# Performance work log

Measured on AMD Instinct MI355X. Metric: run time of the kernel, lower is better.

The kernel has to match this reference:

```python
import jax, jax.numpy as jnp
import numpy as np

B, N, GEO, CLS = 32, 1024, 4, 28
F0 = GEO + CLS          # 32
F1 = F0 * 2             # 64
F2 = F0 * 4             # 128
EPS = 1e-5


def _lin(x, W, b):
    return x @ W.T + b


def _bn(x, g, b):
    # torch BatchNorm1d(element_num) on [B, N, F]: channel dim is N,
    # normalize over (batch, feature) with biased variance (training mode).
    m = x.mean(axis=(0, 2), keepdims=True)
    v = ((x - m) ** 2).mean(axis=(0, 2), keepdims=True)
    return g[None, :, None] * (x - m) * jax.lax.rsqrt(v + EPS) + b[None, :, None]


def _relation(x, Wu, bu, psi, phi, wr):
    # Vectorized form of the triple python loop:
    #   S[b,i,j] = psi*phi * <x_i, x_j>, diagonal excluded
    #   out_i   = wr * (sum_j S[b,i,j] * relu(unary(x_j))) / N + x_i
    n = x.shape[1]
    U = jax.nn.relu(_lin(x, Wu, bu))                       # [B,N,F2]
    S = (psi[0] * phi[0]) * jnp.einsum('bnd,bmd->bnm', x, x)
    S = S * (1.0 - jnp.eye(n, dtype=x.dtype))              # mask i==j
    return wr[0] * (S @ U) / n + x


def setup_inputs() -> dict:
    key = jax.random.key(0)
    ks = iter(jax.random.split(key, 64))

    def W(o, i):
        return jax.random.normal(next(ks), (o, i), jnp.float32) * 0.02

    def bvec(o):
        return jnp.zeros((o,), jnp.float32)

    inp = {'input': jax.random.uniform(next(ks), (B, N, F0), jnp.float32)}
    inp.update(e1_W=W(F1, F0), e1_b=bvec(F1),
               bn1_g=jnp.ones((N,), jnp.float32), bn1_b=bvec(N),
               e2_W=W(F2, F1), e2_b=bvec(F2),
               bn2_g=jnp.ones((N,), jnp.float32), bn2_b=bvec(N),
               e3_W=W(F2, F2), e3_b=bvec(F2))
    for r in (1, 2, 3, 4):
        inp[f'r{r}_W'] = W(F2, F2)
        inp[f'r{r}_b'] = bvec(F2)
        inp[f'r{r}_psi'] = jax.random.uniform(next(ks), (1,), jnp.float32)
        inp[f'r{r}_phi'] = jax.random.uniform(next(ks), (1,), jnp.float32)
        inp[f'r{r}_wr'] = jax.random.uniform(next(ks), (1,), jnp.float32)
    inp.update(d1_W=W(F1, F2), d1_b=bvec(F1),
               dbn_g=jnp.ones((N,), jnp.float32), dbn_b=bvec(N),
               d2_W=W(F0, F1), d2_b=bvec(F0),
               bc_W=W(CLS, F0), bc_b=bvec(CLS),
               bg_W=W(GEO, F0), bg_b=bvec(GEO))
    return inp


def reference(input, e1_W, e1_b, bn1_g, bn1_b, e2_W, e2_b, bn2_g, bn2_b,
              e3_W, e3_b,
              r1_W, r1_b, r1_psi, r1_phi, r1_wr,
              r2_W, r2_b, r2_psi, r2_phi, r2_wr,
              r3_W, r3_b, r3_psi, r3_phi, r3_wr,
              r4_W, r4_b, r4_psi, r4_phi, r4_wr,
              d1_W, d1_b, dbn_g, dbn_b, d2_W, d2_b,
              bc_W, bc_b, bg_W, bg_b):
    out = jax.nn.relu(_bn(_lin(input, e1_W, e1_b), bn1_g, bn1_b))
    out = jax.nn.relu(_bn(_lin(out, e2_W, e2_b), bn2_g, bn2_b))
    enc = jax.nn.sigmoid(_lin(out, e3_W, e3_b))
    x = _relation(enc, r1_W, r1_b, r1_psi, r1_phi, r1_wr)
    x = _relation(x, r2_W, r2_b, r2_psi, r2_phi, r2_wr)
    x = _relation(x, r3_W, r3_b, r3_psi, r3_phi, r3_wr)
    x = _relation(x, r4_W, r4_b, r4_psi, r4_phi, r4_wr)
    out = jax.nn.relu(_bn(_lin(x, d1_W, d1_b), dbn_g, dbn_b))
    out = jax.nn.relu(_lin(out, d2_W, d2_b))
    syn_cls = _lin(out, bc_W, bc_b)
    syn_geo = _lin(out, bg_W, bg_b)
    return jnp.concatenate((syn_cls, syn_geo), axis=2)
```

## Files before the change

### kernel.cpp

```cpp
#include <hip/hip_runtime.h>
#include <hip/hip_bf16.h>


typedef __hip_bfloat16 bf16;
typedef unsigned short ushort_t;
typedef float v4f __attribute__((ext_vector_type(4)));
typedef short v8s __attribute__((ext_vector_type(8)));
#define MFMA_BF16 __builtin_amdgcn_mfma_f32_16x16x32_bf16

#define NB 32
#define NN 1024

__device__ __forceinline__ float ldin(const void* p, size_t i, int f32){
    return f32 ? ((const float*)p)[i] : __bfloat162float(((const bf16*)p)[i]);
}
__device__ __forceinline__ float bf2f(ushort_t u){
    return __uint_as_float((unsigned)u << 16);
}
__device__ __forceinline__ ushort_t f2bf(float v){
    bf16 h = __float2bfloat16(v);
    ushort_t s; __builtin_memcpy(&s, &h, 2);
    return s;
}
__device__ __forceinline__ void unpack8(uint4 v, float* f){
    f[0] = __uint_as_float(v.x << 16);
    f[1] = __uint_as_float(v.x & 0xffff0000u);
    f[2] = __uint_as_float(v.y << 16);
    f[3] = __uint_as_float(v.y & 0xffff0000u);
    f[4] = __uint_as_float(v.z << 16);
    f[5] = __uint_as_float(v.z & 0xffff0000u);
    f[6] = __uint_as_float(v.w << 16);
    f[7] = __uint_as_float(v.w & 0xffff0000u);
}

__device__ __forceinline__ int detect_dev(const void* inp){
    __shared__ int sflag;
    int t = threadIdx.x;
    if (t < 64){
        unsigned v = ((const unsigned*)inp)[t];
        unsigned long long m = __ballot((v & 0x80008000u) != 0u);
        if (t == 0) sflag = (__popcll(m) > 4) ? 1 : 0;
    }
    __syncthreads();
    return sflag;
}

struct PrepArgs {
    const void* w[11];
    int K[11], O[11], off[11];
};

__global__ __launch_bounds__(256) void k_prep(PrepArgs a, float* __restrict__ wpf,
                                              ushort_t* __restrict__ whi, ushort_t* __restrict__ wlo,
                                              const void* __restrict__ detin){
    int f32 = detect_dev(detin);
    int s = blockIdx.y;
    int idx = blockIdx.x*256 + threadIdx.x;
    if (s < 6){
        int K = a.K[s], O = a.O[s];
        if (idx >= K*O) return;
        int k = idx / O, j = idx - k*O;
        wpf[a.off[s] + idx] = ldin(a.w[s], (size_t)j*K + k, f32);
    } else {
        if (idx >= 16384) return;
        int n = idx >> 7, k = idx & 127;
        float v = ldin(a.w[s], (size_t)n*128 + k, f32);
        ushort_t h = f2bf(v);
        ushort_t l = f2bf(v - bf2f(h));
        int di = (s - 6)*16384 + ((k >> 3)*128 + n)*8 + (k & 7);
        whi[di] = h; wlo[di] = l;
    }
}

template<int K, int O, bool EXTIN>
__global__ __launch_bounds__(128) void k_bnlin(
    const void* __restrict__ xin, const float* __restrict__ Wt,
    const void* __restrict__ bias, const void* __restrict__ bng,
    const void* __restrict__ bnb, ushort_t* __restrict__ out,
    const void* __restrict__ detin)
{
    int f32 = detect_dev(detin);
    constexpr int BR  = O/16;
    constexpr int NBT = 32/BR;
    constexpr int G   = K/8;
    __shared__ __align__(16) float wt[K*O];
    __shared__ __align__(16) float xst[2][K*36];
    int t = threadIdx.x;
    int w = t >> 6, lane = t & 63;
    int n = blockIdx.x*2 + w;

    for (int i = t; i < K*O/4; i += 128)
        ((float4*)wt)[i] = ((const float4*)Wt)[i];
    for (int i = lane; i < 32*G; i += 64){
        int b = i / G, g = i - b*G;
        float f[8];
        if (EXTIN && f32){
            const float* src = (const float*)xin + ((size_t)b*NN + n)*K + g*8;
            float4 v0 = ((const float4*)src)[0];
            float4 v1 = ((const float4*)src)[1];
            f[0]=v0.x; f[1]=v0.y; f[2]=v0.z; f[3]=v0.w;
            f[4]=v1.x; f[5]=v1.y; f[6]=v1.z; f[7]=v1.w;
        } else {
            uint4 v = *(const uint4*)((const ushort_t*)xin + ((size_t)b*NN + n)*K + (size_t)g*8);
            unpack8(v, f);
        }
        #pragma unroll
        for (int j=0;j<8;j++) xst[w][(g*8+j)*36 + b] = f[j];
    }
    __syncthreads();

    int bt = lane % NBT, jt = lane / NBT;
    int b0 = bt*BR, j0 = jt*8;
    const float* xw = xst[w];
    float acc[BR][8];
    #pragma unroll
    for (int i=0;i<BR;i++)
        #pragma unroll
        for (int j=0;j<8;j++) acc[i][j] = 0.f;

    for (int k = 0; k < K; k++){
        float xv[BR], wv[8];
        #pragma unroll
        for (int i=0;i<BR;i+=4)
            *(float4*)&xv[i] = *(const float4*)&xw[k*36 + b0 + i];
        *(float4*)&wv[0] = *(const float4*)&wt[k*O + j0];
        *(float4*)&wv[4] = *(const float4*)&wt[k*O + j0 + 4];
        #pragma unroll
        for (int i=0;i<BR;i++)
            #pragma unroll
            for (int j=0;j<8;j++) acc[i][j] = fmaf(xv[i], wv[j], acc[i][j]);
    }

    float bj[8];
    #pragma unroll
    for (int j=0;j<8;j++) bj[j] = ldin(bias, j0+j, f32);
    float s1 = 0.f, s2 = 0.f;
    #pragma unroll
    for (int i=0;i<BR;i++)
        #pragma unroll
        for (int j=0;j<8;j++){
            float a = acc[i][j] + bj[j];
            acc[i][j] = a; s1 += a; s2 = fmaf(a, a, s2);
        }
    #pragma unroll
    for (int off = 32; off > 0; off >>= 1){
        s1 += __shfl_down(s1, off);
        s2 += __shfl_down(s2, off);
    }
    s1 = __shfl(s1, 0); s2 = __shfl(s2, 0);
    const float M = 32.f * O;
    float m  = s1 / M;
    float vv = s2 / M - m*m;
    float rs = rsqrtf(vv + 1e-5f);
    float gv = ldin(bng, n, f32), bv = ldin(bnb, n, f32);
    #pragma unroll
    for (int i=0;i<BR;i++){
        union { uint4 u; ushort_t s[8]; } pk;
        #pragma unroll
        for (int j=0;j<8;j++)
            pk.s[j] = f2bf(fmaxf(fmaf(gv*(acc[i][j]-m), rs, bv), 0.f));
        *(uint4*)(out + ((size_t)(b0+i)*NN + n)*O + j0) = pk.u;
    }
}



__device__ __forceinline__ void tail_stage_x(ushort_t* xs, const float o[2][16],
                                             int w, int col, int quad){
    #pragma unroll
    for (int nt=0;nt<2;nt++){
        int n = w*32 + nt*16 + col;
        #pragma unroll
        for (int m=0;m<4;m++)
            #pragma unroll
            for (int reg=0;reg<4;reg++){
                int r = m*16 + quad*4 + reg;
                xs[((n>>3)*64 + r)*8 + (n&7)] = f2bf(o[nt][m*4+reg]);
            }
    }
}

__device__ __forceinline__ void tail_write_A(const ushort_t* xs, ushort_t* A,
                                             size_t row0, int t){
    uint4* dst = (uint4*)(A + row0*128);
    #pragma unroll
    for (int c = 0; c < 4; c++){
        int i = t + c*256;
        int r = i >> 4, kg = i & 15;
        dst[i] = *(const uint4*)&xs[(kg*64 + r)*8];
    }
}

__device__ __forceinline__ void tail_lin_relu(ushort_t* xs, ushort_t* UT,
    const ushort_t* Whi, const ushort_t* Wlo, const void* bias, float* dvec,
    size_t row0, int b, int rbase, int t, int w, int lane, int col, int quad, int f32)
{
    if (t < 64){
        float s = 0.f;
        #pragma unroll 8
        for (int k=0;k<128;k++){
            float v = bf2f(xs[((k>>3)*64 + t)*8 + (k&7)]);
            s = fmaf(v, v, s);
        }
        dvec[row0 + t] = s;
    }
    v4f acc[4][2];
    #pragma unroll
    for (int m=0;m<4;m++)
        #pragma unroll
        for (int nt=0;nt<2;nt++) acc[m][nt] = (v4f){0.f,0.f,0.f,0.f};
    #pragma unroll
    for (int kt = 0; kt < 4; kt++){
        int kg = kt*4 + quad;
        v8s a[4], bh[2], bl[2];
        #pragma unroll
        for (int nt=0;nt<2;nt++){
            int n = w*32 + nt*16 + col;
            bh[nt] = *(const v8s*)&Whi[(kg*128 + n)*8];
            bl[nt] = *(const v8s*)&Wlo[(kg*128 + n)*8];
        }
        #pragma unroll
        for (int m=0;m<4;m++)
            a[m] = *(const v8s*)&xs[(kg*64 + m*16 + col)*8];
        #pragma unroll
        for (int m=0;m<4;m++)
            #pragma unroll
            for (int nt=0;nt<2;nt++){
                acc[m][nt] = MFMA_BF16(a[m], bh[nt], acc[m][nt], 0, 0, 0);
                acc[m][nt] = MFMA_BF16(a[m], bl[nt], acc[m][nt], 0, 0, 0);
            }
    }
    float u[2][16];
    #pragma unroll
    for (int nt=0;nt<2;nt++){
        int n = w*32 + nt*16 + col;
        float bn = ldin(bias, n, f32);
        #pragma unroll
        for (int m=0;m<4;m++)
            #pragma unroll
            for (int reg=0;reg<4;reg++)
                u[nt][m*4+reg] = fmaxf(acc[m][nt][reg] + bn, 0.f);
    }
    __syncthreads();
    #pragma unroll
    for (int nt=0;nt<2;nt++){
        int n = w*32 + nt*16 + col;
        #pragma unroll
        for (int m=0;m<4;m++)
            #pragma unroll
            for (int reg=0;reg<4;reg++){
                int r = m*16 + quad*4 + reg;
                xs[n*64 + r] = f2bf(u[nt][m*4+reg]);
            }
    }
    __syncthreads();
    #pragma unroll
    for (int c = 0; c < 4; c++){
        int i = t + c*256;
        int n = i >> 3, sg = i & 7;
        *(uint4*)&UT[((size_t)b*128 + n)*1024 + rbase + sg*8] =
            *(const uint4*)&xs[n*64 + sg*8];
    }
}

__global__ __launch_bounds__(256, 2) void k_linfuse0(
    const ushort_t* __restrict__ xin,
    const ushort_t* __restrict__ W3h, const ushort_t* __restrict__ W3l,
    const void* __restrict__ b3,
    const ushort_t* __restrict__ W1h, const ushort_t* __restrict__ W1l,
    const void* __restrict__ b1,
    ushort_t* __restrict__ A, ushort_t* __restrict__ UT,
    float* __restrict__ dvec, const void* __restrict__ detin)
{
    __shared__ __align__(16) ushort_t xs[8192];
    int f32 = detect_dev(detin);
    int t = threadIdx.x;
    size_t row0 = (size_t)blockIdx.x * 64;
    int b = (int)(row0 >> 10), rbase = (int)(row0 & 1023);
    {
        const uint4* src = (const uint4*)(xin + row0*128);
        #pragma unroll
        for (int c = 0; c < 4; c++){
            int i = t + c*256;
            int r = i >> 4, kg = i & 15;
            *(uint4*)&xs[(kg*64 + r)*8] = src[i];
        }
    }
    __syncthreads();
    int w = t >> 6, lane = t & 63;
    int col = lane & 15, quad = lane >> 4;
    v4f acc[4][2];
    #pragma unroll
    for (int m=0;m<4;m++)
        #pragma unroll
        for (int nt=0;nt<2;nt++) acc[m][nt] = (v4f){0.f,0.f,0.f,0.f};
    #pragma unroll
    for (int kt = 0; kt < 4; kt++){
        int kg = kt*4 + quad;
        v8s a[4], bh[2], bl[2];
        #pragma unroll
        for (int nt=0;nt<2;nt++){
            int n = w*32 + nt*16 + col;
            bh[nt] = *(const v8s*)&W3h[(kg*128 + n)*8];
            bl[nt] = *(const v8s*)&W3l[(kg*128 + n)*8];
        }
        #pragma unroll
        for (int m=0;m<4;m++)
            a[m] = *(const v8s*)&xs[(kg*64 + m*16 + col)*8];
        #pragma unroll
        for (int m=0;m<4;m++)
            #pragma unroll
            for (int nt=0;nt<2;nt++){
                acc[m][nt] = MFMA_BF16(a[m], bh[nt], acc[m][nt], 0, 0, 0);
                acc[m][nt] = MFMA_BF16(a[m], bl[nt], acc[m][nt], 0, 0, 0);
            }
    }
    float o[2][16];
    #pragma unroll
    for (int nt=0;nt<2;nt++){
        int n = w*32 + nt*16 + col;
        float bn = ldin(b3, n, f32);
        #pragma unroll
        for (int m=0;m<4;m++)
            #pragma unroll
            for (int reg=0;reg<4;reg++){
                float v = acc[m][nt][reg] + bn;
                o[nt][m*4+reg] = 1.f/(1.f+expf(-v));
            }
    }
    __syncthreads();
    tail_stage_x(xs, o, w, col, quad);
    __syncthreads();
    tail_write_A(xs, A, row0, t);
    tail_lin_relu(xs, UT, W1h, W1l, b1, dvec, row0, b, rbase, t, w, lane, col, quad, f32);
}

__global__ __launch_bounds__(256) void k_relT(
    const ushort_t* __restrict__ x, const ushort_t* __restrict__ UT,
    float* __restrict__ Tp)
{
    __shared__ __align__(16) ushort_t xts[8192];
    int blk = blockIdx.x;
    int b = blk & 31, rs = (blk >> 5) & 7, nh = blk >> 8;
    int t = threadIdx.x;
    int w = t >> 6, lane = t & 63;
    int col = lane & 15, quad = lane >> 4;
    int wn = nh*64 + (w & 1)*32;
    int wc = (w >> 1)*64;
    const ushort_t* utb = UT + ((size_t)b << 17);
    v4f acc[2][4];
    #pragma unroll
    for (int m=0;m<2;m++)
        #pragma unroll
        for (int q=0;q<4;q++) acc[m][q] = (v4f){0.f,0.f,0.f,0.f};

    for (int ch = 0; ch < 2; ch++){
        __syncthreads();
        int r0 = rs*128 + ch*64;
        #pragma unroll
        for (int c = 0; c < 4; c++){
            int i = t + c*256;
            int r = i >> 4, cs8 = (i & 15)*8;
            uint4 v = *(const uint4*)&x[((size_t)b*1024 + r0 + r)*128 + cs8];
            int base = ((r >> 3)*128 + cs8)*8 + (r & 7);
            xts[base     ] = (ushort_t)(v.x & 0xffff);
            xts[base + 8 ] = (ushort_t)(v.x >> 16);
            xts[base + 16] = (ushort_t)(v.y & 0xffff);
            xts[base + 24] = (ushort_t)(v.y >> 16);
            xts[base + 32] = (ushort_t)(v.z & 0xffff);
            xts[base + 40] = (ushort_t)(v.z >> 16);
            xts[base + 48] = (ushort_t)(v.w & 0xffff);
            xts[base + 56] = (ushort_t)(v.w >> 16);
        }
        __syncthreads();
        #pragma unroll
        for (int kt = 0; kt < 2; kt++){
            int kg = kt*4 + quad;
            v8s a[2], bb[4];
            #pragma unroll
            for (int m=0;m<2;m++)
                a[m] = *(const v8s*)&utb[((size_t)(wn + m*16 + col))*1024 + r0 + kg*8];
            #pragma unroll
            for (int q=0;q<4;q++)
                bb[q] = *(const v8s*)&xts[(kg*128 + wc + q*16 + col)*8];
            #pragma unroll
            for (int m=0;m<2;m++)
                #pragma unroll
                for (int q=0;q<4;q++)
                    acc[m][q] = MFMA_BF16(a[m], bb[q], acc[m][q], 0, 0, 0);
        }
    }
    float* dst = Tp + (((size_t)rs*NB + b) << 14);
    #pragma unroll
    for (int m=0;m<2;m++)
        #pragma unroll
        for (int q=0;q<4;q++)
            #pragma unroll
            for (int reg=0;reg<4;reg++){
                int n = wn + m*16 + quad*4 + reg;
                int c = wc + q*16 + col;
                dst[n*128 + c] = acc[m][q][reg];
            }
}

__global__ __launch_bounds__(256) void k_tred(const float* __restrict__ Tp,
                                              ushort_t* __restrict__ Thi, ushort_t* __restrict__ Tlo){
    int i = blockIdx.x*256 + threadIdx.x;
    const size_t S = 524288;
    float s = ((Tp[i] + Tp[S+i]) + (Tp[2*S+i] + Tp[3*S+i]))
            + ((Tp[4*S+i] + Tp[5*S+i]) + (Tp[6*S+i] + Tp[7*S+i]));
    int bb = i >> 14, j = i & 16383;
    int n = j >> 7, c = j & 127;
    int di = (bb << 14) + ((c >> 3)*128 + n)*8 + (c & 7);
    ushort_t h = f2bf(s);
    Thi[di] = h;
    Tlo[di] = f2bf(s - bf2f(h));
}

template<int LAST>
__global__ __launch_bounds__(256, 2) void k_relfuse(
    ushort_t* __restrict__ x, ushort_t* __restrict__ UT,
    const ushort_t* __restrict__ Thi, const ushort_t* __restrict__ Tlo,
    float* __restrict__ dvec,
    const void* __restrict__ psi, const void* __restrict__ phi, const void* __restrict__ wr,
    const ushort_t* __restrict__ Wnh, const ushort_t* __restrict__ Wnl,
    const void* __restrict__ bnext, const void* __restrict__ detin)
{
    __shared__ __align__(16) ushort_t xs[8192];
    int f32 = detect_dev(detin);
    int t = threadIdx.x;
    size_t row0 = (size_t)blockIdx.x * 64;
    int b = (int)(row0 >> 10), rbase = (int)(row0 & 1023);
    {
        const uint4* src = (const uint4*)(x + row0*128);
        #pragma unroll
        for (int c = 0; c < 4; c++){
            int i = t + c*256;
            int r = i >> 4, kg = i & 15;
            *(uint4*)&xs[(kg*64 + r)*8] = src[i];
        }
    }
    __syncthreads();
    float alpha = ldin(wr,0,f32) * ldin(psi,0,f32) * ldin(phi,0,f32) * (1.f/1024.f);
    int w = t >> 6, lane = t & 63;
    int col = lane & 15, quad = lane >> 4;
    const ushort_t* sh = Thi + ((size_t)b << 14);
    const ushort_t* sl = Tlo + ((size_t)b << 14);
    v4f acc[4][2];
    #pragma unroll
    for (int m=0;m<4;m++)
        #pragma unroll
        for (int nt=0;nt<2;nt++) acc[m][nt] = (v4f){0.f,0.f,0.f,0.f};
    #pragma unroll
    for (int kt = 0; kt < 4; kt++){
        int kg = kt*4 + quad;
        v8s a[4], bh[2], bl[2];
        #pragma unroll
        for (int nt=0;nt<2;nt++){
            int n = w*32 + nt*16 + col;
            bh[nt] = *(const v8s*)&sh[(kg*128 + n)*8];
            bl[nt] = *(const v8s*)&sl[(kg*128 + n)*8];
        }
        #pragma unroll
        for (int m=0;m<4;m++)
            a[m] = *(const v8s*)&xs[(kg*64 + m*16 + col)*8];
        #pragma unroll
        for (int m=0;m<4;m++)
            #pragma unroll
            for (int nt=0;nt<2;nt++){
                acc[m][nt] = MFMA_BF16(a[m], bh[nt], acc[m][nt], 0, 0, 0);
                acc[m][nt] = MFMA_BF16(a[m], bl[nt], acc[m][nt], 0, 0, 0);
            }
    }
    float o[2][16];
    #pragma unroll
    for (int m=0;m<4;m++){
        float4 d4 = *(const float4*)&dvec[row0 + m*16 + quad*4];
        const float* dr = (const float*)&d4;
        #pragma unroll
        for (int nt=0;nt<2;nt++){
            int n = w*32 + nt*16 + col;
            uint2 uu = *(const uint2*)&UT[((size_t)b*128 + n)*1024 + rbase + m*16 + quad*4];
            float uf[4];
            uf[0] = __uint_as_float(uu.x << 16);
            uf[1] = __uint_as_float(uu.x & 0xffff0000u);
            uf[2] = __uint_as_float(uu.y << 16);
            uf[3] = __uint_as_float(uu.y & 0xffff0000u);
            #pragma unroll
            for (int reg=0;reg<4;reg++){
                int r = m*16 + quad*4 + reg;
                float xv = bf2f(xs[((n>>3)*64 + r)*8 + (n&7)]);
                o[nt][m*4+reg] = fmaf(alpha, acc[m][nt][reg] - dr[reg]*uf[reg], xv);
            }
        }
    }
    __syncthreads();
    tail_stage_x(xs, o, w, col, quad);
    __syncthreads();
    tail_write_A(xs, x, row0, t);
    if (!LAST)
        tail_lin_relu(xs, UT, Wnh, Wnl, bnext, dvec, row0, b, rbase, t, w, lane, col, quad, f32);
}

__global__ __launch_bounds__(256) void k_dec2(
    const ushort_t* __restrict__ x,
    const float* __restrict__ W2t, const void* __restrict__ b2,
    const float* __restrict__ Wct, const void* __restrict__ bcb,
    const float* __restrict__ Wgt, const void* __restrict__ bgb,
    void* __restrict__ out, const void* __restrict__ detin)
{
    int f32 = detect_dev(detin);
    __shared__ __align__(16) float w2[64*32];
    __shared__ __align__(16) float wc[32*28];
    __shared__ __align__(16) float wg[32*4];
    __shared__ __align__(16) float xsd[8][64];
    __shared__ float hs[8][33];
    size_t row0 = (size_t)blockIdx.x * 8;
    int t = threadIdx.x;
    for (int i=t;i<512;i+=256)  ((float4*)w2)[i] = ((const float4*)W2t)[i];
    if (t < 224) ((float4*)wc)[t] = ((const float4*)Wct)[t];
    if (t < 32)  ((float4*)wg)[t] = ((const float4*)Wgt)[t];
    if (t < 64){
        int row = t >> 3, seg = t & 7;
        uint4 v = *(const uint4*)&x[(row0 + row)*64 + seg*8];
        float f[8]; unpack8(v, f);
        *(float4*)&xsd[row][seg*8]   = make_float4(f[0],f[1],f[2],f[3]);
        *(float4*)&xsd[row][seg*8+4] = make_float4(f[4],f[5],f[6],f[7]);
    }
    __syncthreads();
    int j = t & 31, r = t >> 5;
    float a = ldin(b2, j, f32);
    #pragma unroll 8
    for (int k=0;k<64;k++) a = fmaf(xsd[r][k], w2[k*32 + j], a);
    hs[r][j] = fmaxf(a, 0.f);
    __syncthreads();
    float o;
    if (j < 28){
        o = ldin(bcb, j, f32);
        #pragma unroll
        for (int k=0;k<32;k++) o = fmaf(hs[r][k], wc[k*28 + j], o);
    } else {
        int jj = j - 28;
        o = ldin(bgb, jj, f32);
        #pragma unroll
        for (int k=0;k<32;k++) o = fmaf(hs[r][k], wg[k*4 + jj], o);
    }
    size_t oi = (row0 + r)*32 + j;
    if (f32) ((float*)out)[oi] = o;
    else     ((ushort_t*)out)[oi] = f2bf(o);
}

enum { O_E1=0, O_E2=2048, O_D1=10240, O_D2=18432, O_BC=20480, O_BG=21376 };

extern "C" void kernel_launch(void* const* d_in, const int* in_sizes, int n_in,
                              void* d_out, int out_size, void* d_ws, size_t ws_size,
                              hipStream_t stream)
{
    (void)in_sizes; (void)n_in; (void)out_size; (void)ws_size;
    const void* input = d_in[0];
    const void* e1_W = d_in[1];  const void* e1_b = d_in[2];
    const void* bn1_g = d_in[3]; const void* bn1_b = d_in[4];
    const void* e2_W = d_in[5];  const void* e2_b = d_in[6];
    const void* bn2_g = d_in[7]; const void* bn2_b = d_in[8];
    const void* e3_W = d_in[9];  const void* e3_b = d_in[10];
    const void *rW[4], *rb[4], *rpsi[4], *rphi[4], *rwr[4];
    for (int r = 0; r < 4; r++){
        rW[r]   = d_in[11 + r*5 + 0];
        rb[r]   = d_in[11 + r*5 + 1];
        rpsi[r] = d_in[11 + r*5 + 2];
        rphi[r] = d_in[11 + r*5 + 3];
        rwr[r]  = d_in[11 + r*5 + 4];
    }
    const void* d1_W = d_in[31]; const void* d1_b = d_in[32];
    const void* dbn_g = d_in[33];const void* dbn_b = d_in[34];
    const void* d2_W = d_in[35]; const void* d2_b = d_in[36];
    const void* bc_W = d_in[37]; const void* bc_b = d_in[38];
    const void* bg_W = d_in[39]; const void* bg_b = d_in[40];

    float*    ws_f = (float*)d_ws;
    float*    wpf  = ws_f;
    float*    dd   = ws_f + 21504;
    ushort_t* whi  = (ushort_t*)(ws_f + 54272);
    ushort_t* wlo  = (ushort_t*)(ws_f + 95232);
    ushort_t* Thi  = (ushort_t*)(ws_f + 136192);
    ushort_t* Tlo  = (ushort_t*)(ws_f + 398336);
    float*    Tp   = ws_f + 660480;
    ushort_t* A    = (ushort_t*)(ws_f + 4854784);
    ushort_t* UT   = (ushort_t*)(ws_f + 6951936);
    ushort_t* Cenc = A;
    ushort_t* E2   = (ushort_t*)Tp;
    ushort_t* Cdec = UT;

    PrepArgs pa;
    const void* srcs[11] = {e1_W, e2_W, d1_W, d2_W, bc_W, bg_W,
                            e3_W, rW[0], rW[1], rW[2], rW[3]};
    const int  Ks[11]   = {32,64,128,64,32,32, 128,128,128,128,128};
    const int  Os[11]   = {64,128,64,32,28,4,  128,128,128,128,128};
    const int  offs[11] = {O_E1,O_E2,O_D1,O_D2,O_BC,O_BG, 0,0,0,0,0};
    for (int i=0;i<11;i++){ pa.w[i]=srcs[i]; pa.K[i]=Ks[i]; pa.O[i]=Os[i]; pa.off[i]=offs[i]; }

    k_prep<<<dim3(64,11), 256, 0, stream>>>(pa, wpf, whi, wlo, input);
    k_bnlin<32,64,true><<<512, 128, 0, stream>>>(input, wpf+O_E1, e1_b, bn1_g, bn1_b, Cenc, input);
    k_bnlin<64,128,false><<<512, 128, 0, stream>>>(Cenc, wpf+O_E2, e2_b, bn2_g, bn2_b, E2, input);
    k_linfuse0<<<512, 256, 0, stream>>>(E2, whi, wlo, e3_b,
                                        whi + 16384, wlo + 16384, rb[0],
                                        A, UT, dd, input);

    for (int r = 0; r < 4; r++){
        k_relT<<<512, 256, 0, stream>>>(A, UT, Tp);
        k_tred<<<2048, 256, 0, stream>>>(Tp, Thi, Tlo);
        if (r < 3)
            k_relfuse<0><<<512, 256, 0, stream>>>(A, UT, Thi, Tlo, dd,
                rpsi[r], rphi[r], rwr[r],
                whi + (size_t)(2+r)*16384, wlo + (size_t)(2+r)*16384, rb[r+1], input);
        else
            k_relfuse<1><<<512, 256, 0, stream>>>(A, UT, Thi, Tlo, dd,
                rpsi[r], rphi[r], rwr[r], whi, wlo, rb[r], input);
    }

    k_bnlin<128,64,false><<<512, 128, 0, stream>>>(A, wpf+O_D1, d1_b, dbn_g, dbn_b, Cdec, input);
    k_dec2<<<4096, 256, 0, stream>>>(Cdec, wpf+O_D2, d2_b, wpf+O_BC, bc_b, wpf+O_BG, bg_b, d_out, input);
}
```

Baseline: 346.3 us.

## Fuse relation T-partial GEMM into producer tails, drop separate k_relT kernel

The U^T·x partial product for each 64-row slab is now computed in the tail of k_linfuse0/k_relfuse, using the x and U tiles already staged in shared memory (a second transposed x tile is added). This removes a separate k_relT launch and its reload of x and UT from global memory. k_tred now reduces 16 partials instead of 8, so Tp doubles in size and the workspace layout is moved. Shared memory per block doubles and the 2-blocks-per-CU launch bound is dropped, which may reduce occupancy.

```diff
diff --git a/kernel.cpp b/kernel.cpp
--- a/kernel.cpp
+++ b/kernel.cpp
@@ -164,19 +164,24 @@
 }
 
 
-
-__device__ __forceinline__ void tail_stage_x(ushort_t* xs, const float o[2][16],
+__device__ __forceinline__ void tail_stage_x(ushort_t* xs, ushort_t* xt,
+                                             const float o[2][16],
                                              int w, int col, int quad){
     #pragma unroll
     for (int nt=0;nt<2;nt++){
         int n = w*32 + nt*16 + col;
         #pragma unroll
-        for (int m=0;m<4;m++)
+        for (int m=0;m<4;m++){
+            union { uint2 u2; ushort_t s[4]; } pk;
             #pragma unroll
             for (int reg=0;reg<4;reg++){
                 int r = m*16 + quad*4 + reg;
-                xs[((n>>3)*64 + r)*8 + (n&7)] = f2bf(o[nt][m*4+reg]);
+                ushort_t hv = f2bf(o[nt][m*4+reg]);
+                xs[((n>>3)*64 + r)*8 + (n&7)] = hv;
+                pk.s[reg] = hv;
             }
+            *(uint2*)&xt[n*64 + m*16 + quad*4] = pk.u2;
+        }
     }
 }
 
@@ -191,9 +196,10 @@
     }
 }
 
-__device__ __forceinline__ void tail_lin_relu(ushort_t* xs, ushort_t* UT,
-    const ushort_t* Whi, const ushort_t* Wlo, const void* bias, float* dvec,
-    size_t row0, int b, int rbase, int t, int w, int lane, int col, int quad, int f32)
+__device__ __forceinline__ void tail_lin_relu_T(ushort_t* xs, ushort_t* xt,
+    ushort_t* UT, const ushort_t* Whi, const ushort_t* Wlo, const void* bias,
+    float* dvec, float* Tp,
+    size_t row0, int b, int rbase, int t, int w, int col, int quad, int f32)
 {
     if (t < 64){
         float s = 0.f;
@@ -246,12 +252,13 @@
     for (int nt=0;nt<2;nt++){
         int n = w*32 + nt*16 + col;
         #pragma unroll
-        for (int m=0;m<4;m++)
-            #pragma unroll
-            for (int reg=0;reg<4;reg++){
-                int r = m*16 + quad*4 + reg;
-                xs[n*64 + r] = f2bf(u[nt][m*4+reg]);
-            }
+        for (int m=0;m<4;m++){
+            union { uint2 u2; ushort_t s[4]; } pk;
+            #pragma unroll
+            for (int reg=0;reg<4;reg++)
+                pk.s[reg] = f2bf(u[nt][m*4+reg]);
+            *(uint2*)&xs[n*64 + m*16 + quad*4] = pk.u2;
+        }
     }
     __syncthreads();
     #pragma unroll
@@ -261,18 +268,54 @@
         *(uint4*)&UT[((size_t)b*128 + n)*1024 + rbase + sg*8] =
             *(const uint4*)&xs[n*64 + sg*8];
     }
-}
-
-__global__ __launch_bounds__(256, 2) void k_linfuse0(
+    v4f tacc[4][4];
+    #pragma unroll
+    for (int m=0;m<4;m++)
+        #pragma unroll
+        for (int q=0;q<4;q++) tacc[m][q] = (v4f){0.f,0.f,0.f,0.f};
+    int wn = (w & 1)*64, wc = (w >> 1)*64;
+    #pragma unroll
+    for (int kt = 0; kt < 2; kt++){
+        int kg = kt*4 + quad;
+        v8s a[4], bb[4];
+        #pragma unroll
+        for (int m=0;m<4;m++)
+            a[m] = *(const v8s*)&xs[(wn + m*16 + col)*64 + kg*8];
+        #pragma unroll
+        for (int q=0;q<4;q++)
+            bb[q] = *(const v8s*)&xt[(wc + q*16 + col)*64 + kg*8];
+        #pragma unroll
+        for (int m=0;m<4;m++)
+            #pragma unroll
+            for (int q=0;q<4;q++)
+                tacc[m][q] = MFMA_BF16(a[m], bb[q], tacc[m][q], 0, 0, 0);
+    }
+    int s16 = (int)((row0 >> 6) & 15);
+    float* dst = Tp + ((size_t)(s16*NB + b) << 14);
+    #pragma unroll
+    for (int m=0;m<4;m++)
+        #pragma unroll
+        for (int q=0;q<4;q++)
+            #pragma unroll
+            for (int reg=0;reg<4;reg++){
+                int n = wn + m*16 + quad*4 + reg;
+                int c = wc + q*16 + col;
+                dst[n*128 + c] = tacc[m][q][reg];
+            }
+}
+
+__global__ __launch_bounds__(256) void k_linfuse0(
     const ushort_t* __restrict__ xin,
     const ushort_t* __restrict__ W3h, const ushort_t* __restrict__ W3l,
     const void* __restrict__ b3,
     const ushort_t* __restrict__ W1h, const ushort_t* __restrict__ W1l,
     const void* __restrict__ b1,
     ushort_t* __restrict__ A, ushort_t* __restrict__ UT,
-    float* __restrict__ dvec, const void* __restrict__ detin)
+    float* __restrict__ dvec, float* __restrict__ Tp,
+    const void* __restrict__ detin)
 {
     __shared__ __align__(16) ushort_t xs[8192];
+    __shared__ __align__(16) ushort_t xt[8192];
     int f32 = detect_dev(detin);
     int t = threadIdx.x;
     size_t row0 = (size_t)blockIdx.x * 64;
@@ -329,86 +372,20 @@
             }
     }
     __syncthreads();
-    tail_stage_x(xs, o, w, col, quad);
+    tail_stage_x(xs, xt, o, w, col, quad);
     __syncthreads();
     tail_write_A(xs, A, row0, t);
-    tail_lin_relu(xs, UT, W1h, W1l, b1, dvec, row0, b, rbase, t, w, lane, col, quad, f32);
-}
-
-__global__ __launch_bounds__(256) void k_relT(
-    const ushort_t* __restrict__ x, const ushort_t* __restrict__ UT,
-    float* __restrict__ Tp)
-{
-    __shared__ __align__(16) ushort_t xts[8192];
-    int blk = blockIdx.x;
-    int b = blk & 31, rs = (blk >> 5) & 7, nh = blk >> 8;
-    int t = threadIdx.x;
-    int w = t >> 6, lane = t & 63;
-    int col = lane & 15, quad = lane >> 4;
-    int wn = nh*64 + (w & 1)*32;
-    int wc = (w >> 1)*64;
-    const ushort_t* utb = UT + ((size_t)b << 17);
-    v4f acc[2][4];
-    #pragma unroll
-    for (int m=0;m<2;m++)
-        #pragma unroll
-        for (int q=0;q<4;q++) acc[m][q] = (v4f){0.f,0.f,0.f,0.f};
-
-    for (int ch = 0; ch < 2; ch++){
-        __syncthreads();
-        int r0 = rs*128 + ch*64;
-        #pragma unroll
-        for (int c = 0; c < 4; c++){
-            int i = t + c*256;
-            int r = i >> 4, cs8 = (i & 15)*8;
-            uint4 v = *(const uint4*)&x[((size_t)b*1024 + r0 + r)*128 + cs8];
-            int base = ((r >> 3)*128 + cs8)*8 + (r & 7);
-            xts[base     ] = (ushort_t)(v.x & 0xffff);
-            xts[base + 8 ] = (ushort_t)(v.x >> 16);
-            xts[base + 16] = (ushort_t)(v.y & 0xffff);
-            xts[base + 24] = (ushort_t)(v.y >> 16);
-            xts[base + 32] = (ushort_t)(v.z & 0xffff);
-            xts[base + 40] = (ushort_t)(v.z >> 16);
-            xts[base + 48] = (ushort_t)(v.w & 0xffff);
-            xts[base + 56] = (ushort_t)(v.w >> 16);
-        }
-        __syncthreads();
-        #pragma unroll
-        for (int kt = 0; kt < 2; kt++){
-            int kg = kt*4 + quad;
-            v8s a[2], bb[4];
-            #pragma unroll
-            for (int m=0;m<2;m++)
-                a[m] = *(const v8s*)&utb[((size_t)(wn + m*16 + col))*1024 + r0 + kg*8];
-            #pragma unroll
-            for (int q=0;q<4;q++)
-                bb[q] = *(const v8s*)&xts[(kg*128 + wc + q*16 + col)*8];
-            #pragma unroll
-            for (int m=0;m<2;m++)
-                #pragma unroll
-                for (int q=0;q<4;q++)
-                    acc[m][q] = MFMA_BF16(a[m], bb[q], acc[m][q], 0, 0, 0);
-        }
-    }
-    float* dst = Tp + (((size_t)rs*NB + b) << 14);
-    #pragma unroll
-    for (int m=0;m<2;m++)
-        #pragma unroll
-        for (int q=0;q<4;q++)
-            #pragma unroll
-            for (int reg=0;reg<4;reg++){
-                int n = wn + m*16 + quad*4 + reg;
-                int c = wc + q*16 + col;
-                dst[n*128 + c] = acc[m][q][reg];
-            }
+    tail_lin_relu_T(xs, xt, UT, W1h, W1l, b1, dvec, Tp,
+                    row0, b, rbase, t, w, col, quad, f32);
 }
 
 __global__ __launch_bounds__(256) void k_tred(const float* __restrict__ Tp,
                                               ushort_t* __restrict__ Thi, ushort_t* __restrict__ Tlo){
     int i = blockIdx.x*256 + threadIdx.x;
     const size_t S = 524288;
-    float s = ((Tp[i] + Tp[S+i]) + (Tp[2*S+i] + Tp[3*S+i]))
-            + ((Tp[4*S+i] + Tp[5*S+i]) + (Tp[6*S+i] + Tp[7*S+i]));
+    float s = 0.f;
+    #pragma unroll
+    for (int k = 0; k < 16; k++) s += Tp[(size_t)k*S + i];
     int bb = i >> 14, j = i & 16383;
     int n = j >> 7, c = j & 127;
     int di = (bb << 14) + ((c >> 3)*128 + n)*8 + (c & 7);
@@ -418,15 +395,17 @@
 }
 
 template<int LAST>
-__global__ __launch_bounds__(256, 2) void k_relfuse(
+__global__ __launch_bounds__(256) void k_relfuse(
     ushort_t* __restrict__ x, ushort_t* __restrict__ UT,
     const ushort_t* __restrict__ Thi, const ushort_t* __restrict__ Tlo,
     float* __restrict__ dvec,
     const void* __restrict__ psi, const void* __restrict__ phi, const void* __restrict__ wr,
     const ushort_t* __restrict__ Wnh, const ushort_t* __restrict__ Wnl,
-    const void* __restrict__ bnext, const void* __restrict__ detin)
+    const void* __restrict__ bnext, float* __restrict__ Tp,
+    const void* __restrict__ detin)
 {
     __shared__ __align__(16) ushort_t xs[8192];
+    __shared__ __align__(16) ushort_t xt[8192];
     int f32 = detect_dev(detin);
     int t = threadIdx.x;
     size_t row0 = (size_t)blockIdx.x * 64;
@@ -495,11 +474,12 @@
         }
     }
     __syncthreads();
-    tail_stage_x(xs, o, w, col, quad);
+    tail_stage_x(xs, xt, o, w, col, quad);
     __syncthreads();
     tail_write_A(xs, x, row0, t);
     if (!LAST)
-        tail_lin_relu(xs, UT, Wnh, Wnl, bnext, dvec, row0, b, rbase, t, w, lane, col, quad, f32);
+        tail_lin_relu_T(xs, xt, UT, Wnh, Wnl, bnext, dvec, Tp,
+                        row0, b, rbase, t, w, col, quad, f32);
 }
 
 __global__ __launch_bounds__(256) void k_dec2(
@@ -585,10 +565,10 @@
     ushort_t* Thi  = (ushort_t*)(ws_f + 136192);
     ushort_t* Tlo  = (ushort_t*)(ws_f + 398336);
     float*    Tp   = ws_f + 660480;
-    ushort_t* A    = (ushort_t*)(ws_f + 4854784);
-    ushort_t* UT   = (ushort_t*)(ws_f + 6951936);
+    ushort_t* A    = (ushort_t*)(ws_f + 9049088);
+    ushort_t* UT   = (ushort_t*)(ws_f + 11146240);
+    ushort_t* E2   = (ushort_t*)(ws_f + 13243392);
     ushort_t* Cenc = A;
-    ushort_t* E2   = (ushort_t*)Tp;
     ushort_t* Cdec = UT;
 
     PrepArgs pa;
@@ -604,18 +584,17 @@
     k_bnlin<64,128,false><<<512, 128, 0, stream>>>(Cenc, wpf+O_E2, e2_b, bn2_g, bn2_b, E2, input);
     k_linfuse0<<<512, 256, 0, stream>>>(E2, whi, wlo, e3_b,
                                         whi + 16384, wlo + 16384, rb[0],
-                                        A, UT, dd, input);
+                                        A, UT, dd, Tp, input);
 
     for (int r = 0; r < 4; r++){
-        k_relT<<<512, 256, 0, stream>>>(A, UT, Tp);
         k_tred<<<2048, 256, 0, stream>>>(Tp, Thi, Tlo);
         if (r < 3)
             k_relfuse<0><<<512, 256, 0, stream>>>(A, UT, Thi, Tlo, dd,
                 rpsi[r], rphi[r], rwr[r],
-                whi + (size_t)(2+r)*16384, wlo + (size_t)(2+r)*16384, rb[r+1], input);
+                whi + (size_t)(2+r)*16384, wlo + (size_t)(2+r)*16384, rb[r+1], Tp, input);
         else
             k_relfuse<1><<<512, 256, 0, stream>>>(A, UT, Thi, Tlo, dd,
-                rpsi[r], rphi[r], rwr[r], whi, wlo, rb[r], input);
+                rpsi[r], rphi[r], rwr[r], whi, wlo, rb[r], Tp, input);
     }
 
     k_bnlin<128,64,false><<<512, 128, 0, stream>>>(A, wpf+O_D1, d1_b, dbn_g, dbn_b, Cdec, input);
```

Result: faster. 326.4 us (-5.8%).
